# Optimization experiments

Measured on AMD Instinct MI355X. Metric: run time of the kernel, lower is better.

The kernel has to match this reference:

```python
import jax, jax.numpy as jnp
import numpy as np

EPS = 1e-8


def setup_inputs() -> dict:
    key = jax.random.key(0)
    k1, k2 = jax.random.split(key)
    a = jax.random.normal(k1, (1, 256, 128, 128), dtype=jnp.float32)
    b = jax.random.normal(k2, (1, 256, 128, 128), dtype=jnp.float32)
    return {"a": a, "b": b}


def reference(a, b):
    # a: [n, c, h, w] rendered feats; b: [n, c, h2, w2] style feats (n == 1)
    n, c, h, w = a.shape
    a_flat = a.reshape(n, c, -1)            # [n, c, hw]
    b_flat = b.reshape(n, c, -1)            # [n, c, h2w2]

    # argmin_cos_distance: channel-wise L2 normalize, cosine distance, argmin
    b_norm = jnp.sqrt((b_flat * b_flat).sum(1, keepdims=True) + EPS)
    b_n = b_flat / (b_norm + EPS)
    a_norm = jnp.sqrt((a_flat * a_flat).sum(1, keepdims=True) + EPS)
    a_n = a_flat / (a_norm + EPS)
    d_mat = 1.0 - jnp.einsum('ncp,ncq->npq', a_n, b_n)   # [n, hw, h2w2]
    z_best = jnp.argmin(d_mat, axis=2)                    # [n, hw]

    # nn_feat_replace: gather matched (unnormalized) style features
    idx = jnp.broadcast_to(z_best[:, None, :], b_flat.shape)
    target = jnp.take_along_axis(b_flat, idx, axis=2).reshape(n, c, h, w)

    # cos_loss(a, target): cosine distance over channel dim, mean over pixels
    an = jnp.sqrt((a * a).sum(1, keepdims=True))
    tn = jnp.sqrt((target * target).sum(1, keepdims=True))
    cossim = ((a / (an + EPS)) * (target / (tn + EPS))).sum(1)  # [n, h, w]
    return (1.0 - cossim).mean()
```

## Files before the change

### kernel.cpp

```cpp
#include <hip/hip_runtime.h>
#include <stdint.h>

#define EPS 1e-8f

constexpr int HW = 16384;
constexpr int BM = 128;
constexpr int NG = 2048;

typedef __attribute__((ext_vector_type(4))) float floatx4;
typedef __attribute__((ext_vector_type(8))) int   intx8;
typedef unsigned char u8;
typedef unsigned int u32;
typedef unsigned long long u64;

__device__ inline u32 pk4(float x0, float x1, float x2, float x3) {
    int t = __builtin_amdgcn_cvt_pk_fp8_f32(x0, x1, 0, false);
    t = __builtin_amdgcn_cvt_pk_fp8_f32(x2, x3, t, true);
    return (u32)t;
}

__device__ inline float getc(const float4& f, int j) {
    return (j == 0) ? f.x : (j == 1) ? f.y : (j == 2) ? f.z : f.w;
}

__global__ __launch_bounds__(256) void prep_kernel(const float* __restrict__ a,
                                                   const float* __restrict__ b,
                                                   float* __restrict__ sumsq_a,
                                                   float* __restrict__ sumsq_b,
                                                   u8* __restrict__ aF, u8* __restrict__ bF) {
    __shared__ float red[16][65];
    __shared__ float invb_sh[64];
    const int tid = threadIdx.x;
    const int pg = tid & 15, tc = tid >> 4;
    const int p0 = blockIdx.x * 64, pb = pg * 4;
    const int kb = tc >> 3, qg = (tc >> 1) & 3, lo16 = (tc & 1) * 16;

    float4 bv[16];
    float ss0 = 0.f, ss1 = 0.f, ss2 = 0.f, ss3 = 0.f;
    #pragma unroll
    for (int i = 0; i < 16; ++i) {
        bv[i] = *(const float4*)&b[(size_t)(tc * 16 + i) * HW + p0 + pb];
        ss0 += bv[i].x * bv[i].x; ss1 += bv[i].y * bv[i].y;
        ss2 += bv[i].z * bv[i].z; ss3 += bv[i].w * bv[i].w;
    }
    red[tc][pb] = ss0; red[tc][pb + 1] = ss1; red[tc][pb + 2] = ss2; red[tc][pb + 3] = ss3;
    __syncthreads();
    if (tid < 64) {
        float B = 0.f;
        #pragma unroll
        for (int j = 0; j < 16; ++j) B += red[j][tid];
        sumsq_b[p0 + tid] = B;
        invb_sh[tid] = 1.0f / (sqrtf(B + EPS) + EPS);
    }
    __syncthreads();

    #pragma unroll
    for (int j = 0; j < 4; ++j) {
        const int p = p0 + pb + j;
        const int g = p >> 4, rp = (pb + j) & 15;
        const float inv = invb_sh[pb + j];
        int4 W;
        W.x = (int)pk4(getc(bv[0], j) * inv, getc(bv[1], j) * inv, getc(bv[2], j) * inv, getc(bv[3], j) * inv);
        W.y = (int)pk4(getc(bv[4], j) * inv, getc(bv[5], j) * inv, getc(bv[6], j) * inv, getc(bv[7], j) * inv);
        W.z = (int)pk4(getc(bv[8], j) * inv, getc(bv[9], j) * inv, getc(bv[10], j) * inv, getc(bv[11], j) * inv);
        W.w = (int)pk4(getc(bv[12], j) * inv, getc(bv[13], j) * inv, getc(bv[14], j) * inv, getc(bv[15], j) * inv);
        *(int4*)(bF + (((size_t)(g * 2 + kb)) << 11) + (qg * 16 + rp) * 32 + lo16) = W;
    }

    float4 av[16];
    ss0 = ss1 = ss2 = ss3 = 0.f;
    #pragma unroll
    for (int i = 0; i < 16; ++i) {
        av[i] = *(const float4*)&a[(size_t)(tc * 16 + i) * HW + p0 + pb];
        ss0 += av[i].x * av[i].x; ss1 += av[i].y * av[i].y;
        ss2 += av[i].z * av[i].z; ss3 += av[i].w * av[i].w;
    }
    #pragma unroll
    for (int j = 0; j < 4; ++j) {
        const int p = p0 + pb + j;
        const int g = p >> 4, rp = (pb + j) & 15;
        int4 W;
        W.x = (int)pk4(getc(av[0], j), getc(av[1], j), getc(av[2], j), getc(av[3], j));
        W.y = (int)pk4(getc(av[4], j), getc(av[5], j), getc(av[6], j), getc(av[7], j));
        W.z = (int)pk4(getc(av[8], j), getc(av[9], j), getc(av[10], j), getc(av[11], j));
        W.w = (int)pk4(getc(av[12], j), getc(av[13], j), getc(av[14], j), getc(av[15], j));
        *(int4*)(aF + (((size_t)(g * 2 + kb)) << 11) + (qg * 16 + rp) * 32 + lo16) = W;
    }
    red[tc][pb] = ss0; red[tc][pb + 1] = ss1; red[tc][pb + 2] = ss2; red[tc][pb + 3] = ss3;
    __syncthreads();
    if (tid < 64) {
        float A = 0.f;
        #pragma unroll
        for (int j = 0; j < 16; ++j) A += red[j][tid];
        sumsq_a[p0 + tid] = A;
    }
}

__global__ __launch_bounds__(256, 2) void gemm_argmax(const u8* __restrict__ aF,
                                                      const u8* __restrict__ bF,
                                                      u64* __restrict__ packed) {
    const int tid = threadIdx.x;
    const int w = tid >> 6, lane = tid & 63;
    const int q4 = lane >> 4, r15 = lane & 15;
    const int wm = w >> 1, wn = w & 1;

    const u32 bid = blockIdx.x;
    const u32 ng = bid & 7;
    const u32 mt = bid >> 3;
    const int p0 = (int)mt * BM;

    const u8* gA = aF + (((size_t)(mt * 8 + wm * 4)) << 12) + (u32)lane * 32;
    intx8 Afr[4][2];
    #pragma unroll
    for (int mi = 0; mi < 4; ++mi)
        #pragma unroll
        for (int kb = 0; kb < 2; ++kb)
            Afr[mi][kb] = *(const intx8*)(gA + (u32)(mi * 2 + kb) * 2048u);

    const u8* gB = bF + (((size_t)(ng * 128 + wn * 2)) << 12) + (u32)lane * 32;

    double best[4][4];
    #pragma unroll
    for (int mi = 0; mi < 4; ++mi)
        #pragma unroll
        for (int r = 0; r < 4; ++r) best[mi][r] = 0.0;

    const u32 qlane = ng * 2048 + wn * 32 + (u32)r15;
    const floatx4 C64 = {64.f, 64.f, 64.f, 64.f};
    const int SCL = 0x7F7F7F7F;

    intx8 Bfr[2][2];
    #pragma unroll
    for (int ni = 0; ni < 2; ++ni)
        Bfr[0][ni] = *(const intx8*)(gB + (u32)ni * 4096u);

    for (int qt = 0; qt < 32; ++qt) {
        const u32 qo = (u32)qt * 16384u;
        floatx4 acc[4][2];
        #pragma unroll
        for (int ni = 0; ni < 2; ++ni)
            Bfr[1][ni] = *(const intx8*)(gB + qo + (u32)ni * 4096u + 2048u);
        #pragma unroll
        for (int mi = 0; mi < 4; ++mi)
            #pragma unroll
            for (int ni = 0; ni < 2; ++ni)
                acc[mi][ni] = __builtin_amdgcn_mfma_scale_f32_16x16x128_f8f6f4(
                    Afr[mi][0], Bfr[0][ni], C64, 0, 0, 0, SCL, 0, SCL);
        const u32 nqo = (qt + 1 < 32) ? qo + 16384u : qo;
        #pragma unroll
        for (int ni = 0; ni < 2; ++ni)
            Bfr[0][ni] = *(const intx8*)(gB + nqo + (u32)ni * 4096u);
        #pragma unroll
        for (int mi = 0; mi < 4; ++mi)
            #pragma unroll
            for (int ni = 0; ni < 2; ++ni)
                acc[mi][ni] = __builtin_amdgcn_mfma_scale_f32_16x16x128_f8f6f4(
                    Afr[mi][1], Bfr[1][ni], acc[mi][ni], 0, 0, 0, SCL, 0, SCL);

        const u32 lo0 = 0xFFFFFFFFu - (qlane + (u32)qt * 64u);
        #pragma unroll
        for (int mi = 0; mi < 4; ++mi)
            #pragma unroll
            for (int ni = 0; ni < 2; ++ni) {
                const u32 lw = lo0 - (u32)(ni * 16);
                #pragma unroll
                for (int r = 0; r < 4; ++r) {
                    u64 pk = ((u64)__float_as_uint(acc[mi][ni][r]) << 32) | (u64)lw;
                    best[mi][r] = fmax(best[mi][r], __longlong_as_double((long long)pk));
                }
            }
    }

    #pragma unroll
    for (int mi = 0; mi < 4; ++mi)
        #pragma unroll
        for (int r = 0; r < 4; ++r) {
            u64 pk = (u64)__double_as_longlong(best[mi][r]);
            #pragma unroll
            for (int d = 1; d < 16; d <<= 1) {
                u64 o = __shfl_xor((unsigned long long)pk, d);
                pk = o > pk ? o : pk;
            }
            if (r15 == 0)
                atomicMax(&packed[p0 + wm * 64 + mi * 16 + q4 * 4 + r], pk);
        }
}

__global__ void loss_kernel(const u64* __restrict__ packed,
                            const float* __restrict__ sumsq_a, const float* __restrict__ sumsq_b,
                            float* __restrict__ out) {
    int p = blockIdx.x * 256 + threadIdx.x;
    u64 pk = packed[p];
    float s = __uint_as_float((u32)(pk >> 32)) - 64.0f;
    u32 q = 0xFFFFFFFFu - (u32)(pk & 0xFFFFFFFFull);
    float A = sumsq_a[p], B = sumsq_b[q];
    float dot = s * (sqrtf(B + EPS) + EPS);
    float cossim = dot / ((sqrtf(A) + EPS) * (sqrtf(B) + EPS));
    float v = (1.0f - cossim) * (1.0f / (float)HW);
    #pragma unroll
    for (int d = 1; d < 64; d <<= 1) v += __shfl_xor(v, d);
    if ((threadIdx.x & 63) == 0) atomicAdd(out, v);
}

extern "C" void kernel_launch(void* const* d_in, const int* in_sizes, int n_in,
                              void* d_out, int out_size, void* d_ws, size_t ws_size,
                              hipStream_t stream) {
    const float* a = (const float*)d_in[0];
    const float* b = (const float*)d_in[1];
    float* out = (float*)d_out;
    char* ws = (char*)d_ws;

    u8*    aF      = (u8*)ws;
    u8*    bF      = (u8*)(ws + (size_t)4 * 1024 * 1024);
    float* sumsq_a = (float*)(ws + (size_t)8 * 1024 * 1024);
    float* sumsq_b = sumsq_a + HW;
    u64*   packed  = (u64*)(sumsq_b + HW);

    hipMemsetAsync(out, 0, sizeof(float), stream);
    hipMemsetAsync(packed, 0, (size_t)HW * sizeof(u64), stream);

    prep_kernel<<<dim3(HW / 64), 256, 0, stream>>>(a, b, sumsq_a, sumsq_b, aF, bF);
    gemm_argmax<<<dim3((HW / BM) * (HW / NG)), 256, 0, stream>>>(aF, bF, packed);
    loss_kernel<<<dim3(HW / 256), 256, 0, stream>>>(packed, sumsq_a, sumsq_b, out);
}
```

Baseline: 163.0 us.

## Replace double-packed argmax with float+index select, reduce B registers, raise occupancy

The GEMM argmax kernel now tracks the best score as a float value plus a u32 index with compare/select, instead of packing both into a double and using fmax. B fragments are cut to two single intx8 registers with interleaved loads, and each MFMA group is wrapped in s_setprio. Launch bounds go from 2 to 3 waves per SIMD to raise occupancy. The prep kernel is also reshaped to 32 pixels per block with 8-byte stores. The lower register budget risks spills, and tie-breaking now relies on the order of the strict greater-than compare plus the final packed reduction.

```diff
diff --git a/kernel.cpp b/kernel.cpp
--- a/kernel.cpp
+++ b/kernel.cpp
@@ -28,27 +28,27 @@
                                                    float* __restrict__ sumsq_a,
                                                    float* __restrict__ sumsq_b,
                                                    u8* __restrict__ aF, u8* __restrict__ bF) {
-    __shared__ float red[16][65];
-    __shared__ float invb_sh[64];
+    __shared__ float red[32][33];
+    __shared__ float invb_sh[32];
     const int tid = threadIdx.x;
-    const int pg = tid & 15, tc = tid >> 4;
-    const int p0 = blockIdx.x * 64, pb = pg * 4;
-    const int kb = tc >> 3, qg = (tc >> 1) & 3, lo16 = (tc & 1) * 16;
-
-    float4 bv[16];
+    const int pg = tid & 7, tc = tid >> 3;
+    const int p0 = blockIdx.x * 32, pb = pg * 4;
+    const int kb = tc >> 4, qg = (tc >> 2) & 3, e0 = (tc & 3) * 8;
+
+    float4 bv[8];
     float ss0 = 0.f, ss1 = 0.f, ss2 = 0.f, ss3 = 0.f;
     #pragma unroll
-    for (int i = 0; i < 16; ++i) {
-        bv[i] = *(const float4*)&b[(size_t)(tc * 16 + i) * HW + p0 + pb];
+    for (int i = 0; i < 8; ++i) {
+        bv[i] = *(const float4*)&b[(size_t)(tc * 8 + i) * HW + p0 + pb];
         ss0 += bv[i].x * bv[i].x; ss1 += bv[i].y * bv[i].y;
         ss2 += bv[i].z * bv[i].z; ss3 += bv[i].w * bv[i].w;
     }
     red[tc][pb] = ss0; red[tc][pb + 1] = ss1; red[tc][pb + 2] = ss2; red[tc][pb + 3] = ss3;
     __syncthreads();
-    if (tid < 64) {
+    if (tid < 32) {
         float B = 0.f;
         #pragma unroll
-        for (int j = 0; j < 16; ++j) B += red[j][tid];
+        for (int j = 0; j < 32; ++j) B += red[j][tid];
         sumsq_b[p0 + tid] = B;
         invb_sh[tid] = 1.0f / (sqrtf(B + EPS) + EPS);
     }
@@ -57,46 +57,42 @@
     #pragma unroll
     for (int j = 0; j < 4; ++j) {
         const int p = p0 + pb + j;
-        const int g = p >> 4, rp = (pb + j) & 15;
+        const int g = p >> 4, rp = p & 15;
         const float inv = invb_sh[pb + j];
-        int4 W;
-        W.x = (int)pk4(getc(bv[0], j) * inv, getc(bv[1], j) * inv, getc(bv[2], j) * inv, getc(bv[3], j) * inv);
-        W.y = (int)pk4(getc(bv[4], j) * inv, getc(bv[5], j) * inv, getc(bv[6], j) * inv, getc(bv[7], j) * inv);
-        W.z = (int)pk4(getc(bv[8], j) * inv, getc(bv[9], j) * inv, getc(bv[10], j) * inv, getc(bv[11], j) * inv);
-        W.w = (int)pk4(getc(bv[12], j) * inv, getc(bv[13], j) * inv, getc(bv[14], j) * inv, getc(bv[15], j) * inv);
-        *(int4*)(bF + (((size_t)(g * 2 + kb)) << 11) + (qg * 16 + rp) * 32 + lo16) = W;
-    }
-
-    float4 av[16];
+        u64 wv = (u64)pk4(getc(bv[0], j) * inv, getc(bv[1], j) * inv,
+                          getc(bv[2], j) * inv, getc(bv[3], j) * inv)
+               | ((u64)pk4(getc(bv[4], j) * inv, getc(bv[5], j) * inv,
+                           getc(bv[6], j) * inv, getc(bv[7], j) * inv) << 32);
+        *(u64*)(bF + (((size_t)(g * 2 + kb)) << 11) + (qg * 16 + rp) * 32 + e0) = wv;
+    }
+
+    float4 av[8];
     ss0 = ss1 = ss2 = ss3 = 0.f;
     #pragma unroll
-    for (int i = 0; i < 16; ++i) {
-        av[i] = *(const float4*)&a[(size_t)(tc * 16 + i) * HW + p0 + pb];
+    for (int i = 0; i < 8; ++i) {
+        av[i] = *(const float4*)&a[(size_t)(tc * 8 + i) * HW + p0 + pb];
         ss0 += av[i].x * av[i].x; ss1 += av[i].y * av[i].y;
         ss2 += av[i].z * av[i].z; ss3 += av[i].w * av[i].w;
     }
     #pragma unroll
     for (int j = 0; j < 4; ++j) {
         const int p = p0 + pb + j;
-        const int g = p >> 4, rp = (pb + j) & 15;
-        int4 W;
-        W.x = (int)pk4(getc(av[0], j), getc(av[1], j), getc(av[2], j), getc(av[3], j));
-        W.y = (int)pk4(getc(av[4], j), getc(av[5], j), getc(av[6], j), getc(av[7], j));
-        W.z = (int)pk4(getc(av[8], j), getc(av[9], j), getc(av[10], j), getc(av[11], j));
-        W.w = (int)pk4(getc(av[12], j), getc(av[13], j), getc(av[14], j), getc(av[15], j));
-        *(int4*)(aF + (((size_t)(g * 2 + kb)) << 11) + (qg * 16 + rp) * 32 + lo16) = W;
+        const int g = p >> 4, rp = p & 15;
+        u64 wv = (u64)pk4(getc(av[0], j), getc(av[1], j), getc(av[2], j), getc(av[3], j))
+               | ((u64)pk4(getc(av[4], j), getc(av[5], j), getc(av[6], j), getc(av[7], j)) << 32);
+        *(u64*)(aF + (((size_t)(g * 2 + kb)) << 11) + (qg * 16 + rp) * 32 + e0) = wv;
     }
     red[tc][pb] = ss0; red[tc][pb + 1] = ss1; red[tc][pb + 2] = ss2; red[tc][pb + 3] = ss3;
     __syncthreads();
-    if (tid < 64) {
+    if (tid < 32) {
         float A = 0.f;
         #pragma unroll
-        for (int j = 0; j < 16; ++j) A += red[j][tid];
+        for (int j = 0; j < 32; ++j) A += red[j][tid];
         sumsq_a[p0 + tid] = A;
     }
 }
 
-__global__ __launch_bounds__(256, 2) void gemm_argmax(const u8* __restrict__ aF,
+__global__ __launch_bounds__(256, 3) void gemm_argmax(const u8* __restrict__ aF,
                                                       const u8* __restrict__ bF,
                                                       u64* __restrict__ packed) {
     const int tid = threadIdx.x;
@@ -119,63 +115,83 @@
 
     const u8* gB = bF + (((size_t)(ng * 128 + wn * 2)) << 12) + (u32)lane * 32;
 
-    double best[4][4];
+    float bestv[4][4];
+    u32   bestq[4][4];
     #pragma unroll
     for (int mi = 0; mi < 4; ++mi)
         #pragma unroll
-        for (int r = 0; r < 4; ++r) best[mi][r] = 0.0;
-
-    const u32 qlane = ng * 2048 + wn * 32 + (u32)r15;
+        for (int r = 0; r < 4; ++r) { bestv[mi][r] = -3.4e38f; bestq[mi][r] = 0; }
+
+    u32 q0 = ng * 2048 + wn * 32 + (u32)r15;
     const floatx4 C64 = {64.f, 64.f, 64.f, 64.f};
     const int SCL = 0x7F7F7F7F;
 
-    intx8 Bfr[2][2];
-    #pragma unroll
-    for (int ni = 0; ni < 2; ++ni)
-        Bfr[0][ni] = *(const intx8*)(gB + (u32)ni * 4096u);
+    intx8 B0 = *(const intx8*)gB;
+    intx8 B1;
 
     for (int qt = 0; qt < 32; ++qt) {
-        const u32 qo = (u32)qt * 16384u;
+        const u8* gq = gB + (u32)qt * 16384u;
         floatx4 acc[4][2];
-        #pragma unroll
-        for (int ni = 0; ni < 2; ++ni)
-            Bfr[1][ni] = *(const intx8*)(gB + qo + (u32)ni * 4096u + 2048u);
+
+        B1 = *(const intx8*)(gq + 4096u);
+        __builtin_amdgcn_s_setprio(1);
+        #pragma unroll
+        for (int mi = 0; mi < 4; ++mi)
+            acc[mi][0] = __builtin_amdgcn_mfma_scale_f32_16x16x128_f8f6f4(
+                Afr[mi][0], B0, C64, 0, 0, 0, SCL, 0, SCL);
+        __builtin_amdgcn_s_setprio(0);
+
+        B0 = *(const intx8*)(gq + 2048u);
+        __builtin_amdgcn_s_setprio(1);
+        #pragma unroll
+        for (int mi = 0; mi < 4; ++mi)
+            acc[mi][1] = __builtin_amdgcn_mfma_scale_f32_16x16x128_f8f6f4(
+                Afr[mi][0], B1, C64, 0, 0, 0, SCL, 0, SCL);
+        __builtin_amdgcn_s_setprio(0);
+
+        B1 = *(const intx8*)(gq + 6144u);
+        __builtin_amdgcn_s_setprio(1);
+        #pragma unroll
+        for (int mi = 0; mi < 4; ++mi)
+            acc[mi][0] = __builtin_amdgcn_mfma_scale_f32_16x16x128_f8f6f4(
+                Afr[mi][1], B0, acc[mi][0], 0, 0, 0, SCL, 0, SCL);
+        __builtin_amdgcn_s_setprio(0);
+
+        B0 = *(const intx8*)(gB + (u32)((qt + 1) & 31) * 16384u);
+        __builtin_amdgcn_s_setprio(1);
+        #pragma unroll
+        for (int mi = 0; mi < 4; ++mi)
+            acc[mi][1] = __builtin_amdgcn_mfma_scale_f32_16x16x128_f8f6f4(
+                Afr[mi][1], B1, acc[mi][1], 0, 0, 0, SCL, 0, SCL);
+        __builtin_amdgcn_s_setprio(0);
+
         #pragma unroll
         for (int mi = 0; mi < 4; ++mi)
             #pragma unroll
-            for (int ni = 0; ni < 2; ++ni)
-                acc[mi][ni] = __builtin_amdgcn_mfma_scale_f32_16x16x128_f8f6f4(
-                    Afr[mi][0], Bfr[0][ni], C64, 0, 0, 0, SCL, 0, SCL);
-        const u32 nqo = (qt + 1 < 32) ? qo + 16384u : qo;
-        #pragma unroll
-        for (int ni = 0; ni < 2; ++ni)
-            Bfr[0][ni] = *(const intx8*)(gB + nqo + (u32)ni * 4096u);
+            for (int r = 0; r < 4; ++r) {
+                float v = acc[mi][0][r];
+                bool gt = v > bestv[mi][r];
+                bestv[mi][r] = gt ? v : bestv[mi][r];
+                bestq[mi][r] = gt ? q0 : bestq[mi][r];
+            }
         #pragma unroll
         for (int mi = 0; mi < 4; ++mi)
             #pragma unroll
-            for (int ni = 0; ni < 2; ++ni)
-                acc[mi][ni] = __builtin_amdgcn_mfma_scale_f32_16x16x128_f8f6f4(
-                    Afr[mi][1], Bfr[1][ni], acc[mi][ni], 0, 0, 0, SCL, 0, SCL);
-
-        const u32 lo0 = 0xFFFFFFFFu - (qlane + (u32)qt * 64u);
-        #pragma unroll
-        for (int mi = 0; mi < 4; ++mi)
-            #pragma unroll
-            for (int ni = 0; ni < 2; ++ni) {
-                const u32 lw = lo0 - (u32)(ni * 16);
-                #pragma unroll
-                for (int r = 0; r < 4; ++r) {
-                    u64 pk = ((u64)__float_as_uint(acc[mi][ni][r]) << 32) | (u64)lw;
-                    best[mi][r] = fmax(best[mi][r], __longlong_as_double((long long)pk));
-                }
+            for (int r = 0; r < 4; ++r) {
+                float v = acc[mi][1][r];
+                bool gt = v > bestv[mi][r];
+                bestv[mi][r] = gt ? v : bestv[mi][r];
+                bestq[mi][r] = gt ? (q0 + 16u) : bestq[mi][r];
             }
+        q0 += 64u;
     }
 
     #pragma unroll
     for (int mi = 0; mi < 4; ++mi)
         #pragma unroll
         for (int r = 0; r < 4; ++r) {
-            u64 pk = (u64)__double_as_longlong(best[mi][r]);
+            u64 pk = ((u64)__float_as_uint(bestv[mi][r]) << 32)
+                   | (u64)(0xFFFFFFFFu - bestq[mi][r]);
             #pragma unroll
             for (int d = 1; d < 16; d <<= 1) {
                 u64 o = __shfl_xor((unsigned long long)pk, d);
@@ -219,7 +235,7 @@
     hipMemsetAsync(out, 0, sizeof(float), stream);
     hipMemsetAsync(packed, 0, (size_t)HW * sizeof(u64), stream);
 
-    prep_kernel<<<dim3(HW / 64), 256, 0, stream>>>(a, b, sumsq_a, sumsq_b, aF, bF);
+    prep_kernel<<<dim3(HW / 32), 256, 0, stream>>>(a, b, sumsq_a, sumsq_b, aF, bF);
     gemm_argmax<<<dim3((HW / BM) * (HW / NG)), 256, 0, stream>>>(aF, bF, packed);
     loss_kernel<<<dim3(HW / 256), 256, 0, stream>>>(packed, sumsq_a, sumsq_b, out);
 }
```

Measured after the change: 156.6 us. -4.0%, faster.
